# Performance work log

Hardware: AMD Instinct MI355X
Metric: run time of the kernel (lower is better)

The kernel has to match this reference:

```python
import jax, jax.numpy as jnp
import numpy as np

B, S, HID, NH, HD, RD = 1, 2048, 2560, 32, 80, 64
SCALE = HD ** -0.5
NEG = -1e9


def _alibi_slopes(n):
    # n = 32 is a power of two -> standard geometric slopes 2^(-8i/n)
    return jnp.asarray(2.0 ** (-8.0 * np.arange(1, n + 1) / n), dtype=jnp.float32)


def _rope(x, pos):
    # GPT-NeoX style rotary on the first RD dims of each head; x: [B,S,NH,HD]
    inv_freq = 1.0 / (10000.0 ** (np.arange(0, RD, 2, dtype=np.float32) / RD))  # [RD/2]
    ang = pos.astype(jnp.float32)[..., None] * jnp.asarray(inv_freq)  # [B,S,RD/2]
    cos = jnp.cos(ang)[:, :, None, :]  # [B,S,1,RD/2]
    sin = jnp.sin(ang)[:, :, None, :]
    x1 = x[..., : RD // 2]
    x2 = x[..., RD // 2 : RD]
    rot = jnp.concatenate([x1 * cos - x2 * sin, x2 * cos + x1 * sin], axis=-1)
    return jnp.concatenate([rot, x[..., RD:]], axis=-1)


def setup_inputs() -> dict:
    key = jax.random.key(0)
    k1, k2, k3 = jax.random.split(key, 3)
    return {
        "position_ids": jnp.arange(B * S, dtype=jnp.int32).reshape(B, S) % S,
        "hidden_states": jax.random.normal(k1, (B, S, HID), dtype=jnp.float32),
        "w_qkv": jax.random.normal(k2, (HID, 3 * HID), dtype=jnp.float32) * 0.02,
        "w_out": jax.random.normal(k3, (HID, HID), dtype=jnp.float32) * 0.02,
    }


def reference(position_ids, hidden_states, w_qkv, w_out):
    qkv = hidden_states @ w_qkv                       # [B,S,3*HID]
    q, k, v = jnp.split(qkv, 3, axis=-1)
    q = _rope(q.reshape(B, S, NH, HD), position_ids)
    k = _rope(k.reshape(B, S, NH, HD), position_ids)
    v = v.reshape(B, S, NH, HD)

    scores = jnp.einsum("bqhd,bkhd->bhqk", q, k) * SCALE  # [B,NH,S,S]
    rel = (position_ids[:, None, :] - position_ids[:, :, None]).astype(jnp.float32)  # j - i
    slopes = _alibi_slopes(NH)
    bias = slopes[None, :, None, None] * rel[:, None, :, :]  # [B,NH,S,S]
    causal = rel <= 0.0
    scores = jnp.where(causal[:, None, :, :], scores + bias, NEG)
    attn = jax.nn.softmax(scores, axis=-1)
    out = jnp.einsum("bhqk,bkhd->bqhd", attn, v).reshape(B, S, HID)
    return out @ w_out
```

## Files before the change

kernel.cpp:

```cpp
#include <hip/hip_runtime.h>
#include <type_traits>
#include <utility>

typedef unsigned short u16;
typedef unsigned int u32;
typedef __attribute__((ext_vector_type(8))) short short8;
typedef __attribute__((ext_vector_type(8))) __bf16 bhalf8;
typedef __attribute__((ext_vector_type(4))) short short4v;
typedef __attribute__((ext_vector_type(4))) __bf16 bhalf4;
typedef __attribute__((ext_vector_type(4))) float f32x4;
typedef __attribute__((ext_vector_type(4))) unsigned short us4;

#define S_LEN 2048
#define NHEAD 32
#define HD 80
#define HDP 96
#define HID 2560
#define N3 7680
#define QK_SCALE 0.11180339887498949f
#define LOG2E 1.4426950408889634f

template <typename T, typename = void> struct MfmaTakes : std::false_type {};
template <typename T>
struct MfmaTakes<T, std::void_t<decltype(__builtin_amdgcn_mfma_f32_16x16x32_bf16(
                       std::declval<T>(), std::declval<T>(), std::declval<f32x4>(), 0, 0, 0))>>
    : std::true_type {};

template <typename AB>
__device__ inline f32x4 mfma_raw(AB a, AB b, f32x4 c) {
  return __builtin_amdgcn_mfma_f32_16x16x32_bf16(a, b, c, 0, 0, 0);
}
using mfma_ab_t = std::conditional_t<MfmaTakes<bhalf8>::value, bhalf8, short8>;
__device__ inline f32x4 MFMA(short8 a, short8 b, f32x4 c) {
  return mfma_raw<mfma_ab_t>(__builtin_bit_cast(mfma_ab_t, a),
                             __builtin_bit_cast(mfma_ab_t, b), c);
}

#if defined(__has_builtin)
#if __has_builtin(__builtin_amdgcn_mfma_f32_16x16x16bf16_1k)
#define MFMA16_RAW(a, b, c) __builtin_amdgcn_mfma_f32_16x16x16bf16_1k(a, b, c, 0, 0, 0)
#define HAVE_MFMA16 1
#elif __has_builtin(__builtin_amdgcn_mfma_f32_16x16x16_bf16)
#define MFMA16_RAW(a, b, c) __builtin_amdgcn_mfma_f32_16x16x16_bf16(a, b, c, 0, 0, 0)
#define HAVE_MFMA16 1
#endif
#endif

#ifdef HAVE_MFMA16
template <typename T, typename = void> struct M16Takes : std::false_type {};
template <typename T>
struct M16Takes<T, std::void_t<decltype(MFMA16_RAW(std::declval<T>(), std::declval<T>(),
                                                   std::declval<f32x4>()))>> : std::true_type {};
using m16_t = std::conditional_t<M16Takes<bhalf4>::value, bhalf4, short4v>;
__device__ inline f32x4 MFMA16(short4v a, short4v b, f32x4 c) {
  return MFMA16_RAW(__builtin_bit_cast(m16_t, a), __builtin_bit_cast(m16_t, b), c);
}
#else
__device__ inline f32x4 MFMA16(short4v a, short4v b, f32x4 c) {
  short8 a8 = {a[0], a[1], a[2], a[3], 0, 0, 0, 0};
  short8 b8 = {b[0], b[1], b[2], b[3], 0, 0, 0, 0};
  return MFMA(a8, b8, c);
}
#endif

__device__ inline float bf2f(u16 b) { return __uint_as_float(((u32)b) << 16); }
__device__ inline u16 f2bf(float f) {
  u32 u = __float_as_uint(f);
  u += 0x7fffu + ((u >> 16) & 1u);
  return (u16)(u >> 16);
}

typedef __attribute__((address_space(1))) void as1_void;
typedef __attribute__((address_space(3))) void as3_void;

#if defined(__has_builtin)
#if __has_builtin(__builtin_amdgcn_global_load_lds)
#define HAVE_GLL 1
#endif
#endif

__device__ inline void stage16(const u16* g, u16* lds_base, int lane) {
#ifdef HAVE_GLL
  (void)lane;
  __builtin_amdgcn_global_load_lds((as1_void*)g, (as3_void*)lds_base, 16, 0, 0);
#else
  *(short8*)(lds_base + lane * 8) = *(const short8*)g;
#endif
}

__device__ inline void sched_barrier0() {
#if defined(__has_builtin)
#if __has_builtin(__builtin_amdgcn_sched_barrier)
  __builtin_amdgcn_sched_barrier(0);
#endif
#endif
}

__global__ __launch_bounds__(256) void detect_dtype(const u32* __restrict__ words,
                                                    int* __restrict__ flag) {
  __shared__ int red[256];
  int junk = 0;
  for (int i = threadIdx.x; i < 2048; i += 256) {
    u16 lo = (u16)(words[i] & 0xffffu);
    u32 e = (lo >> 7) & 0xffu;
    junk += (e >= 137u);
  }
  red[threadIdx.x] = junk;
  __syncthreads();
  for (int s = 128; s > 0; s >>= 1) {
    if (threadIdx.x < s) red[threadIdx.x] += red[threadIdx.x + s];
    __syncthreads();
  }
  if (threadIdx.x == 0) flag[0] = (red[0] > 64) ? 1 : 0;
}

__global__ __launch_bounds__(256) void convert_hidden(const void* __restrict__ in,
                                                      u16* __restrict__ out, int n4,
                                                      const int* __restrict__ flagp) {
  const int f = *flagp;
  int i = blockIdx.x * 256 + threadIdx.x;
  if (i >= n4) return;
  if (f) {
    const float* inf = (const float*)in;
    us4 o;
#pragma unroll
    for (int j = 0; j < 4; ++j) o[j] = f2bf(inf[(size_t)i * 4 + j]);
    *(us4*)&out[(size_t)i * 4] = o;
  } else {
    *(us4*)&out[(size_t)i * 4] = *(const us4*)&((const u16*)in)[(size_t)i * 4];
  }
}

__global__ __launch_bounds__(256) void transpose64(const void* __restrict__ in,
                                                   u16* __restrict__ out,
                                                   int istride, int ioff, int ostride,
                                                   const int* __restrict__ flagp) {
  __shared__ u16 tile[64][66];
  const int f = flagp ? *flagp : 0;
  const int bx = blockIdx.x * 64, by = blockIdx.y * 64;
  const int tx4 = (threadIdx.x & 15) * 4, ty = threadIdx.x >> 4;
#pragma unroll
  for (int i = 0; i < 4; ++i) {
    const int row = ty + i * 16;
    const size_t idx = (size_t)(by + row) * istride + ioff + bx + tx4;
    us4 v;
    if (f) {
      const f32x4 x = *(const f32x4*)&((const float*)in)[idx];
#pragma unroll
      for (int j = 0; j < 4; ++j) v[j] = f2bf(x[j]);
    } else {
      v = *(const us4*)&((const u16*)in)[idx];
    }
    *(u32*)&tile[row][tx4] = (u32)v[0] | ((u32)v[1] << 16);
    *(u32*)&tile[row][tx4 + 2] = (u32)v[2] | ((u32)v[3] << 16);
  }
  __syncthreads();
#pragma unroll
  for (int i = 0; i < 4; ++i) {
    const int oc = ty + i * 16;
    us4 o;
#pragma unroll
    for (int j = 0; j < 4; ++j) o[j] = tile[tx4 + j][oc];
    *(us4*)&out[(size_t)(bx + oc) * ostride + by + tx4] = o;
  }
}

__global__ __launch_bounds__(256) void gemm_bt(const u16* __restrict__ A,
                                               const u16* __restrict__ Bt,
                                               void* __restrict__ C,
                                               int M, int N, int K,
                                               const int* __restrict__ flagp) {
  __shared__ u16 As[128 * 32];
  __shared__ u16 Bs[128 * 32];
  const int tid = threadIdx.x;
  const int w = tid >> 6, l = tid & 63;
  const int la = l & 15, qd = l >> 4;
  const int m0 = blockIdx.y * 128, n0 = blockIdx.x * 128;
  const int mw = (w >> 1) * 64, nw = (w & 1) * 64;
  const int rowA = l >> 2;
  const int segk = (l & 3) * 8;
  const int of32 = flagp ? *flagp : 0;
  f32x4 acc[4][4] = {};

  for (int k0 = 0; k0 < K; k0 += 32) {
#pragma unroll
    for (int j = 0; j < 2; ++j) {
      const int rb = w * 16 + j * 64;
      const u16* ga = A + (size_t)(m0 + rb + rowA) * K + k0 + segk;
      const u16* gb = Bt + (size_t)(n0 + rb + rowA) * K + k0 + segk;
      stage16(ga, &As[rb * 32], l);
      stage16(gb, &Bs[rb * 32], l);
    }
    __syncthreads();
    short8 af[4], bfr[4];
#pragma unroll
    for (int i = 0; i < 4; ++i)
      af[i] = *(const short8*)&As[(mw + i * 16 + la) * 32 + qd * 8];
#pragma unroll
    for (int j = 0; j < 4; ++j)
      bfr[j] = *(const short8*)&Bs[(nw + j * 16 + la) * 32 + qd * 8];
#pragma unroll
    for (int i = 0; i < 4; ++i)
#pragma unroll
      for (int j = 0; j < 4; ++j)
        acc[i][j] = MFMA(af[i], bfr[j], acc[i][j]);
    __syncthreads();
  }

#pragma unroll
  for (int i = 0; i < 4; ++i)
#pragma unroll
    for (int j = 0; j < 4; ++j) {
      const int r0 = m0 + mw + i * 16 + qd * 4;
      const int c0 = n0 + nw + j * 16 + la;
#pragma unroll
      for (int r = 0; r < 4; ++r) {
        if (of32)
          ((float*)C)[(size_t)(r0 + r) * N + c0] = acc[i][j][r];
        else
          ((u16*)C)[(size_t)(r0 + r) * N + c0] = f2bf(acc[i][j][r]);
      }
    }
}

__global__ __launch_bounds__(512, 2) void gemm256(const u16* __restrict__ A,
                                                  const u16* __restrict__ Bt,
                                                  u16* __restrict__ C,
                                                  int M, int N, int K) {
  __shared__ u16 As[2][256 * 64];
  __shared__ u16 Bs[2][256 * 64];
  const int tid = threadIdx.x;
  const int w = tid >> 6, l = tid & 63, la = l & 15, qd = l >> 4;
  const int wr = w >> 2, wc = w & 3;

  const int nbx = gridDim.x;
  const int nwg = nbx * gridDim.y;
  int lin = blockIdx.y * nbx + blockIdx.x;
  if ((nwg & 7) == 0) lin = (lin & 7) * (nwg >> 3) + (lin >> 3);
  const int m0 = (lin / nbx) * 256, n0 = (lin % nbx) * 256;
  const int NT = K >> 6;

  const int sx0 = (qd ^ (la & 7)) * 8;
  const int sx1 = ((4 + qd) ^ (la & 7)) * 8;
  const int gsw = ((tid & 7) ^ ((tid >> 3) & 7)) * 8;

  f32x4 acc[8][4] = {};

  auto issue = [&](int s) {
    if (s >= NT * 4) return;
    const int kt = s >> 2, part = s & 3, buf = kt & 1;
    const int h = part & 1;
    const u16* G = (part >= 2) ? A : Bt;
    const int b0 = (part >= 2) ? m0 : n0;
    u16* L = ((part >= 2) ? &As[buf][0] : &Bs[buf][0]) + h * 8192;
    const int k0 = kt << 6;
#pragma unroll
    for (int q = 0; q < 2; ++q) {
      const int row = h * 128 + q * 64 + (tid >> 3);
      const u16* g = G + (size_t)(b0 + row) * K + k0 + gsw;
      stage16(g, L + (q * 512 + w * 64) * 8, l);
    }
  };

  auto readA = [&](int buf, int mh, short8(&af)[4][2]) {
    const u16* base = &As[buf][0];
#pragma unroll
    for (int i = 0; i < 4; ++i) {
      const int ro = (wr * 128 + mh * 64 + i * 16 + la) * 64;
      af[i][0] = *(const short8*)(base + ro + sx0);
      af[i][1] = *(const short8*)(base + ro + sx1);
    }
  };
  auto readB = [&](int buf, int nh, short8(&bf)[2][2]) {
    const u16* base = &Bs[buf][0];
#pragma unroll
    for (int j = 0; j < 2; ++j) {
      const int ro = (wc * 64 + nh * 32 + j * 16 + la) * 64;
      bf[j][0] = *(const short8*)(base + ro + sx0);
      bf[j][1] = *(const short8*)(base + ro + sx1);
    }
  };
  auto quad = [&](short8(&af)[4][2], short8(&bf)[2][2], int mh, int nh) {
#pragma unroll
    for (int kk = 0; kk < 2; ++kk)
#pragma unroll
      for (int i = 0; i < 4; ++i)
#pragma unroll
        for (int jj = 0; jj < 2; ++jj)
          acc[mh * 4 + i][nh * 2 + jj] =
              MFMA(af[i][kk], bf[jj][kk], acc[mh * 4 + i][nh * 2 + jj]);
  };

#pragma unroll
  for (int s = 0; s < 6; ++s) issue(s);
  asm volatile("s_waitcnt vmcnt(4)" ::: "memory");
  __builtin_amdgcn_s_barrier();

  for (int t = 0; t < NT; ++t) {
    const int buf = t & 1;
    short8 af[4][2], af2[4][2], bf0[2][2], bf1[2][2];
    readA(buf, 0, af);
    sched_barrier0();
    readB(buf, 0, bf0);
    sched_barrier0();
    readB(buf, 1, bf1);
    sched_barrier0();
    issue(4 * t + 6);
    issue(4 * t + 7);
    asm volatile("s_waitcnt lgkmcnt(4)" ::: "memory");
    sched_barrier0();
    readA(buf, 1, af2);
    sched_barrier0();
    __builtin_amdgcn_s_setprio(1);
    quad(af, bf0, 0, 0);
    __builtin_amdgcn_s_setprio(0);
    asm volatile("s_waitcnt lgkmcnt(8)" ::: "memory");
    sched_barrier0();
    __builtin_amdgcn_s_setprio(1);
    quad(af, bf1, 0, 1);
    __builtin_amdgcn_s_setprio(0);
    __builtin_amdgcn_s_barrier();
    issue(4 * t + 8);
    issue(4 * t + 9);
    asm volatile("s_waitcnt lgkmcnt(0)" ::: "memory");
    sched_barrier0();
    __builtin_amdgcn_s_setprio(1);
    quad(af2, bf0, 1, 0);
    quad(af2, bf1, 1, 1);
    __builtin_amdgcn_s_setprio(0);
    asm volatile("s_waitcnt vmcnt(4)" ::: "memory");
    __builtin_amdgcn_s_barrier();
  }

#pragma unroll
  for (int i = 0; i < 8; ++i)
#pragma unroll
    for (int j = 0; j < 4; ++j) {
      const int r0 = m0 + wr * 128 + i * 16 + qd * 4;
      const int c0 = n0 + wc * 64 + j * 16 + la;
#pragma unroll
      for (int r = 0; r < 4; ++r)
        C[(size_t)(r0 + r) * N + c0] = f2bf(acc[i][j][r]);
    }
}

__global__ __launch_bounds__(256) void rope_prep(const u16* __restrict__ qkv,
                                                 const int* __restrict__ pos,
                                                 u16* __restrict__ Qh,
                                                 u16* __restrict__ Kt) {
  const int s = blockIdx.x;
  const int h = blockIdx.y * 4 + (threadIdx.x >> 6);
  const int t = threadIdx.x & 63;
  const size_t qin = (size_t)s * N3 + h * HD;
  const size_t kin = qin + HID;
  const size_t ob = ((size_t)h * S_LEN + s) * HDP;
  const size_t kb = ((size_t)(h * 32) + (s >> 6)) * 6144 + (size_t)(s & 63) * 8;
  if (t < 32) {
    const float p = (float)pos[s];
    const float inv = exp2f(-(float)t * (13.287712379549449f / 32.0f));
    const float ang = p * inv;
    const float cs = cosf(ang), sn = sinf(ang);
    float x1 = bf2f(qkv[qin + t]), x2 = bf2f(qkv[qin + t + 32]);
    Qh[ob + t] = f2bf(x1 * cs - x2 * sn);
    Qh[ob + t + 32] = f2bf(x2 * cs + x1 * sn);
    x1 = bf2f(qkv[kin + t]);
    x2 = bf2f(qkv[kin + t + 32]);
    Kt[kb + (size_t)(t >> 3) * 512 + (t & 7)] = f2bf(x1 * cs - x2 * sn);
    const int d2 = t + 32;
    Kt[kb + (size_t)(d2 >> 3) * 512 + (d2 & 7)] = f2bf(x2 * cs + x1 * sn);
  } else if (t < 48) {
    const int d = t + 32;
    Qh[ob + d] = qkv[qin + d];
    Kt[kb + (size_t)(d >> 3) * 512 + (d & 7)] = qkv[kin + d];
  } else {
    const int d = t + 32;
    Qh[ob + d] = 0;
    Kt[kb + (size_t)(d >> 3) * 512 + (d & 7)] = 0;
  }
}

__global__ __launch_bounds__(512) void attn_fused(const u16* __restrict__ Qh,
                                                  const u16* __restrict__ Kt,
                                                  const u16* __restrict__ Vt,
                                                  u16* __restrict__ AO) {
  __shared__ u16 Ks[2][768 * 8];
  __shared__ u16 Vs[2][640 * 8];
  const int tid = threadIdx.x, w = tid >> 6, l = tid & 63;
  const int la = l & 15, qd = l >> 4;
  const int h = blockIdx.y;
  const int p = blockIdx.x;
  const int q0A = (15 - p) * 128;
  const int q0B = p * 128;
  const int nItA = (q0A >> 6) + 2;
  const int nItB = (q0B >> 6) + 2;
  const size_t hS = (size_t)h * S_LEN;

  short8 qfA[3], qfB[3];
#pragma unroll
  for (int c = 0; c < 3; ++c) {
    qfA[c] = *(const short8*)&Qh[(hS + q0A + w * 16 + la) * HDP + c * 32 + qd * 8];
    qfB[c] = *(const short8*)&Qh[(hS + q0B + w * 16 + la) * HDP + c * 32 + qd * 8];
  }

  const float slope2 = exp2f(-0.25f * (float)(h + 1)) * LOG2E;
  const float scl2 = QK_SCALE * LOG2E;
  float m_i = -1e30f, l_i = 0.f;
  f32x4 acc[5] = {};

  const u16* gK = Kt + (size_t)h * 32 * 6144;
  const u16* gV = Vt + (size_t)h * HD * S_LEN;

  auto stage = [&](int kt_g, int buf) {
    const u16* gkt = gK + (size_t)kt_g * 6144;
    stage16(gkt + (size_t)(w * 64 + l) * 8, &Ks[buf][(w * 64) * 8], l);
    if (w < 4)
      stage16(gkt + (size_t)(512 + w * 64 + l) * 8, &Ks[buf][(512 + w * 64) * 8], l);
    const u16* gv = gV + (kt_g << 6);
    {
      const int c = w * 64 + l;
      const int row = c >> 3, seg = c & 7;
      const int gcol = ((seg - (row & 7)) & 7) * 8;
      stage16(gv + (size_t)row * S_LEN + gcol, &Vs[buf][(w * 64) * 8], l);
    }
    if (w < 2) {
      const int c = 512 + w * 64 + l;
      const int row = c >> 3, seg = c & 7;
      const int gcol = ((seg - (row & 7)) & 7) * 8;
      stage16(gv + (size_t)row * S_LEN + gcol, &Vs[buf][(512 + w * 64) * 8], l);
    }
  };

  int g = 0;
  stage(0, 0);

  auto run_seg = [&](const short8(&qf)[3], int q0, int nIt, bool more) {
    const int qb = q0 + w * 16;
    const int q = qb + la;
    for (int it = 0; it < nIt; ++it, ++g) {
      const int buf = g & 1;
      __syncthreads();
      if (it + 1 < nIt) stage(it + 1, buf ^ 1);
      else if (more) stage(0, buf ^ 1);
      const int k0 = it << 6;
      if (k0 >= qb + 16) continue;

      f32x4 st[4];
#pragma unroll
      for (int kt = 0; kt < 4; ++kt) {
        short8 kf[3];
#pragma unroll
        for (int c = 0; c < 3; ++c)
          kf[c] = *(const short8*)&Ks[buf][((c * 4 + qd) * 64 + kt * 16 + la) * 8];
        f32x4 z = {};
#pragma unroll
        for (int c = 0; c < 3; ++c) z = MFMA(kf[c], qf[c], z);
        st[kt] = z;
      }

      const float base = (float)(k0 + qd * 4 - q);
      float mloc = -1e30f;
      if (k0 + 64 <= qb + 1) {
#pragma unroll
        for (int kt = 0; kt < 4; ++kt)
#pragma unroll
          for (int r = 0; r < 4; ++r) {
            const float rel = base + (float)(kt * 16 + r);
            const float v = st[kt][r] * scl2 + slope2 * rel;
            st[kt][r] = v;
            mloc = fmaxf(mloc, v);
          }
      } else {
#pragma unroll
        for (int kt = 0; kt < 4; ++kt)
#pragma unroll
          for (int r = 0; r < 4; ++r) {
            const float rel = base + (float)(kt * 16 + r);
            const float v = (rel <= 0.f) ? st[kt][r] * scl2 + slope2 * rel : -1e30f;
            st[kt][r] = v;
            mloc = fmaxf(mloc, v);
          }
      }
      mloc = fmaxf(mloc, __shfl_xor(mloc, 16));
      mloc = fmaxf(mloc, __shfl_xor(mloc, 32));

      if (!__all(mloc - m_i <= 8.0f)) {
        const float nm = fmaxf(m_i, mloc);
        const float al = exp2f(m_i - nm);
        m_i = nm;
        l_i *= al;
#pragma unroll
        for (int dt = 0; dt < 5; ++dt) acc[dt] *= al;
      }

      float ps = 0.f;
      short4v pf[4];
#pragma unroll
      for (int kt = 0; kt < 4; ++kt) {
        short4v pk;
#pragma unroll
        for (int r = 0; r < 4; ++r) {
          const float pv = exp2f(st[kt][r] - m_i);
          ps += pv;
          pk[r] = (short)f2bf(pv);
        }
        pf[kt] = pk;
      }
      ps += __shfl_xor(ps, 16);
      ps += __shfl_xor(ps, 32);
      l_i += ps;

      const int cb = qd * 4 + ((la & 7) << 3);
#pragma unroll
      for (int dt = 0; dt < 5; ++dt) {
        const int vrow = (dt * 16 + la) * 64;
#pragma unroll
        for (int kt = 0; kt < 4; ++kt) {
          const short4v vf = *(const short4v*)&Vs[buf][vrow + ((kt * 16 + cb) & 63)];
          acc[dt] = MFMA16(vf, pf[kt], acc[dt]);
        }
      }
    }
    const float inv = 1.0f / l_i;
    const size_t row = (size_t)q;
#pragma unroll
    for (int dt = 0; dt < 5; ++dt) {
      us4 o;
#pragma unroll
      for (int r = 0; r < 4; ++r) o[r] = f2bf(acc[dt][r] * inv);
      *(us4*)&AO[row * HID + h * HD + dt * 16 + qd * 4] = o;
    }
    m_i = -1e30f;
    l_i = 0.f;
#pragma unroll
    for (int dt = 0; dt < 5; ++dt) acc[dt] = f32x4{};
  };

  run_seg(qfA, q0A, nItA, true);
  run_seg(qfB, q0B, nItB, false);
}

extern "C" void kernel_launch(void* const* d_in, const int* in_sizes, int n_in,
                              void* d_out, int out_size, void* d_ws, size_t ws_size,
                              hipStream_t stream) {
  const int* pos = (const int*)d_in[0];
  const void* hidden = d_in[1];
  const void* w_qkv = d_in[2];
  const void* w_out = d_in[3];
  u16* ws = (u16*)d_ws;

  u16* Hb = ws;
  u16* WtQ = Hb + (size_t)S_LEN * HID;
  u16* WtO = WtQ + (size_t)N3 * HID;
  u16* qkv = WtO + (size_t)HID * HID;
  int* flag = (int*)(qkv + (size_t)S_LEN * N3);
  u16* Vt = Hb;
  u16* Qh = WtQ;
  u16* Kh = Qh + (size_t)NHEAD * S_LEN * HDP;
  u16* AO = Kh + (size_t)NHEAD * S_LEN * HDP;

  detect_dtype<<<1, 256, 0, stream>>>((const u32*)hidden, flag);
  convert_hidden<<<(S_LEN * HID / 4 + 255) / 256, 256, 0, stream>>>(hidden, Hb,
                                                                    S_LEN * HID / 4, flag);
  transpose64<<<dim3(N3 / 64, HID / 64), 256, 0, stream>>>(w_qkv, WtQ, N3, 0, HID, flag);
  transpose64<<<dim3(HID / 64, HID / 64), 256, 0, stream>>>(w_out, WtO, HID, 0, HID, flag);
  gemm256<<<dim3(N3 / 256, S_LEN / 256), 512, 0, stream>>>(Hb, WtQ, qkv, S_LEN, N3, HID);
  transpose64<<<dim3(HID / 64, S_LEN / 64), 256, 0, stream>>>(qkv, Vt, N3, 2 * HID, S_LEN,
                                                              nullptr);
  rope_prep<<<dim3(S_LEN, NHEAD / 4), 256, 0, stream>>>(qkv, pos, Qh, Kh);
  attn_fused<<<dim3(8, NHEAD), 512, 0, stream>>>(Qh, Kh, Vt, AO);
  gemm_bt<<<dim3(HID / 128, S_LEN / 128), 256, 0, stream>>>(AO, WtO, d_out, S_LEN, HID, HID,
                                                            flag);
}
```

Baseline: 426.8 us.

## Pipeline output GEMM with double-buffered LDS and split attention into per-tile blocks

Replaces the simple single-buffered output projection GEMM with a 128x128 kernel that uses 64-wide K tiles, double-buffered swizzled LDS, XCD-aware block remapping, interleaved load issue, and explicit waitcnt/priority scheduling to overlap global loads with MFMA work. The attention kernel no longer pairs two query tiles per block. It launches one block per 128-row tile, with the tile order reversed for half the heads to balance work, and raises the occupancy hint. The intent is better latency hiding in both kernels. The cost is more complex hand scheduling and an uneven causal workload per block.

```diff
diff --git a/kernel.cpp b/kernel.cpp
--- a/kernel.cpp
+++ b/kernel.cpp
@@ -165,54 +165,123 @@
   }
 }
 
-__global__ __launch_bounds__(256) void gemm_bt(const u16* __restrict__ A,
-                                               const u16* __restrict__ Bt,
-                                               void* __restrict__ C,
-                                               int M, int N, int K,
-                                               const int* __restrict__ flagp) {
-  __shared__ u16 As[128 * 32];
-  __shared__ u16 Bs[128 * 32];
+__global__ __launch_bounds__(256, 2) void gemm128c(const u16* __restrict__ A,
+                                                   const u16* __restrict__ Bt,
+                                                   void* __restrict__ C,
+                                                   int M, int N, int K,
+                                                   const int* __restrict__ flagp) {
+  __shared__ u16 As[2][128 * 64];
+  __shared__ u16 Bs[2][128 * 64];
   const int tid = threadIdx.x;
-  const int w = tid >> 6, l = tid & 63;
-  const int la = l & 15, qd = l >> 4;
-  const int m0 = blockIdx.y * 128, n0 = blockIdx.x * 128;
-  const int mw = (w >> 1) * 64, nw = (w & 1) * 64;
-  const int rowA = l >> 2;
-  const int segk = (l & 3) * 8;
+  const int w = tid >> 6, l = tid & 63, la = l & 15, qd = l >> 4;
+  const int wr = w >> 1, wc = w & 1;
   const int of32 = flagp ? *flagp : 0;
+
+  const int nbx = gridDim.x;
+  const int nwg = nbx * gridDim.y;
+  int lin = blockIdx.y * nbx + blockIdx.x;
+  if ((nwg & 7) == 0) lin = (lin & 7) * (nwg >> 3) + (lin >> 3);
+  const int m0 = (lin / nbx) * 128, n0 = (lin % nbx) * 128;
+  const int NT = K >> 6;
+
+  const int sx0 = (qd ^ (la & 7)) * 8;
+  const int sx1 = ((4 + qd) ^ (la & 7)) * 8;
+  const int gsw = ((tid & 7) ^ ((tid >> 3) & 7)) * 8;
+
   f32x4 acc[4][4] = {};
 
-  for (int k0 = 0; k0 < K; k0 += 32) {
+  auto issue = [&](int s) {
+    if (s >= NT * 4) return;
+    const int kt = s >> 2, part = s & 3, buf = kt & 1;
+    const int h = part & 1;
+    const u16* G = (part >= 2) ? A : Bt;
+    const int b0 = (part >= 2) ? m0 : n0;
+    u16* L = ((part >= 2) ? &As[buf][0] : &Bs[buf][0]) + h * 4096;
+    const int k0 = kt << 6;
+#pragma unroll
+    for (int q = 0; q < 2; ++q) {
+      const int row = h * 64 + q * 32 + (tid >> 3);
+      const u16* g = G + (size_t)(b0 + row) * K + k0 + gsw;
+      stage16(g, L + (q * 256 + w * 64) * 8, l);
+    }
+  };
+
+  auto readA = [&](int buf, int mh, short8(&af)[2][2]) {
+    const u16* base = &As[buf][0];
+#pragma unroll
+    for (int i = 0; i < 2; ++i) {
+      const int ro = (wr * 64 + mh * 32 + i * 16 + la) * 64;
+      af[i][0] = *(const short8*)(base + ro + sx0);
+      af[i][1] = *(const short8*)(base + ro + sx1);
+    }
+  };
+  auto readB = [&](int buf, int nh, short8(&bf)[2][2]) {
+    const u16* base = &Bs[buf][0];
 #pragma unroll
     for (int j = 0; j < 2; ++j) {
-      const int rb = w * 16 + j * 64;
-      const u16* ga = A + (size_t)(m0 + rb + rowA) * K + k0 + segk;
-      const u16* gb = Bt + (size_t)(n0 + rb + rowA) * K + k0 + segk;
-      stage16(ga, &As[rb * 32], l);
-      stage16(gb, &Bs[rb * 32], l);
-    }
-    __syncthreads();
-    short8 af[4], bfr[4];
-#pragma unroll
-    for (int i = 0; i < 4; ++i)
-      af[i] = *(const short8*)&As[(mw + i * 16 + la) * 32 + qd * 8];
-#pragma unroll
-    for (int j = 0; j < 4; ++j)
-      bfr[j] = *(const short8*)&Bs[(nw + j * 16 + la) * 32 + qd * 8];
-#pragma unroll
-    for (int i = 0; i < 4; ++i)
-#pragma unroll
-      for (int j = 0; j < 4; ++j)
-        acc[i][j] = MFMA(af[i], bfr[j], acc[i][j]);
-    __syncthreads();
+      const int ro = (wc * 64 + nh * 32 + j * 16 + la) * 64;
+      bf[j][0] = *(const short8*)(base + ro + sx0);
+      bf[j][1] = *(const short8*)(base + ro + sx1);
+    }
+  };
+  auto quad = [&](short8(&af)[2][2], short8(&bf)[2][2], int mh, int nh) {
+#pragma unroll
+    for (int kk = 0; kk < 2; ++kk)
+#pragma unroll
+      for (int i = 0; i < 2; ++i)
+#pragma unroll
+        for (int jj = 0; jj < 2; ++jj)
+          acc[mh * 2 + i][nh * 2 + jj] =
+              MFMA(af[i][kk], bf[jj][kk], acc[mh * 2 + i][nh * 2 + jj]);
+  };
+
+#pragma unroll
+  for (int s = 0; s < 6; ++s) issue(s);
+  asm volatile("s_waitcnt vmcnt(4)" ::: "memory");
+  __builtin_amdgcn_s_barrier();
+
+  for (int t = 0; t < NT; ++t) {
+    const int buf = t & 1;
+    short8 af[2][2], af2[2][2], bf0[2][2], bf1[2][2];
+    readA(buf, 0, af);
+    sched_barrier0();
+    readB(buf, 0, bf0);
+    sched_barrier0();
+    readB(buf, 1, bf1);
+    sched_barrier0();
+    issue(4 * t + 6);
+    issue(4 * t + 7);
+    asm volatile("s_waitcnt lgkmcnt(4)" ::: "memory");
+    sched_barrier0();
+    readA(buf, 1, af2);
+    sched_barrier0();
+    __builtin_amdgcn_s_setprio(1);
+    quad(af, bf0, 0, 0);
+    __builtin_amdgcn_s_setprio(0);
+    asm volatile("s_waitcnt lgkmcnt(4)" ::: "memory");
+    sched_barrier0();
+    __builtin_amdgcn_s_setprio(1);
+    quad(af, bf1, 0, 1);
+    __builtin_amdgcn_s_setprio(0);
+    __builtin_amdgcn_s_barrier();
+    issue(4 * t + 8);
+    issue(4 * t + 9);
+    asm volatile("s_waitcnt lgkmcnt(0)" ::: "memory");
+    sched_barrier0();
+    __builtin_amdgcn_s_setprio(1);
+    quad(af2, bf0, 1, 0);
+    quad(af2, bf1, 1, 1);
+    __builtin_amdgcn_s_setprio(0);
+    asm volatile("s_waitcnt vmcnt(4)" ::: "memory");
+    __builtin_amdgcn_s_barrier();
   }
 
 #pragma unroll
   for (int i = 0; i < 4; ++i)
 #pragma unroll
     for (int j = 0; j < 4; ++j) {
-      const int r0 = m0 + mw + i * 16 + qd * 4;
-      const int c0 = n0 + nw + j * 16 + la;
+      const int r0 = m0 + wr * 64 + (i >> 1) * 32 + (i & 1) * 16 + qd * 4;
+      const int c0 = n0 + wc * 64 + (j >> 1) * 32 + (j & 1) * 16 + la;
 #pragma unroll
       for (int r = 0; r < 4; ++r) {
         if (of32)
@@ -379,28 +448,27 @@
   }
 }
 
-__global__ __launch_bounds__(512) void attn_fused(const u16* __restrict__ Qh,
-                                                  const u16* __restrict__ Kt,
-                                                  const u16* __restrict__ Vt,
-                                                  u16* __restrict__ AO) {
+__global__ __launch_bounds__(512, 4) void attn_fused(const u16* __restrict__ Qh,
+                                                     const u16* __restrict__ Kt,
+                                                     const u16* __restrict__ Vt,
+                                                     u16* __restrict__ AO) {
   __shared__ u16 Ks[2][768 * 8];
   __shared__ u16 Vs[2][640 * 8];
   const int tid = threadIdx.x, w = tid >> 6, l = tid & 63;
   const int la = l & 15, qd = l >> 4;
   const int h = blockIdx.y;
   const int p = blockIdx.x;
-  const int q0A = (15 - p) * 128;
-  const int q0B = p * 128;
-  const int nItA = (q0A >> 6) + 2;
-  const int nItB = (q0B >> 6) + 2;
+  const int tile = (h < 16) ? p : 15 - p;
+  const int q0 = tile * 128;
+  const int nIt = 2 * tile + 2;
   const size_t hS = (size_t)h * S_LEN;
 
-  short8 qfA[3], qfB[3];
-#pragma unroll
-  for (int c = 0; c < 3; ++c) {
-    qfA[c] = *(const short8*)&Qh[(hS + q0A + w * 16 + la) * HDP + c * 32 + qd * 8];
-    qfB[c] = *(const short8*)&Qh[(hS + q0B + w * 16 + la) * HDP + c * 32 + qd * 8];
-  }
+  const int qb = q0 + w * 16;
+  const int q = qb + la;
+  short8 qf[3];
+#pragma unroll
+  for (int c = 0; c < 3; ++c)
+    qf[c] = *(const short8*)&Qh[(hS + qb + la) * HDP + c * 32 + qd * 8];
 
   const float slope2 = exp2f(-0.25f * (float)(h + 1)) * LOG2E;
   const float scl2 = QK_SCALE * LOG2E;
@@ -430,113 +498,100 @@
     }
   };
 
-  int g = 0;
   stage(0, 0);
-
-  auto run_seg = [&](const short8(&qf)[3], int q0, int nIt, bool more) {
-    const int qb = q0 + w * 16;
-    const int q = qb + la;
-    for (int it = 0; it < nIt; ++it, ++g) {
-      const int buf = g & 1;
-      __syncthreads();
-      if (it + 1 < nIt) stage(it + 1, buf ^ 1);
-      else if (more) stage(0, buf ^ 1);
-      const int k0 = it << 6;
-      if (k0 >= qb + 16) continue;
-
-      f32x4 st[4];
+  for (int it = 0; it < nIt; ++it) {
+    const int buf = it & 1;
+    __syncthreads();
+    if (it + 1 < nIt) stage(it + 1, buf ^ 1);
+    const int k0 = it << 6;
+    if (k0 >= qb + 16) continue;
+
+    f32x4 st[4];
+#pragma unroll
+    for (int kt = 0; kt < 4; ++kt) {
+      short8 kf[3];
+#pragma unroll
+      for (int c = 0; c < 3; ++c)
+        kf[c] = *(const short8*)&Ks[buf][((c * 4 + qd) * 64 + kt * 16 + la) * 8];
+      f32x4 z = {};
+#pragma unroll
+      for (int c = 0; c < 3; ++c) z = MFMA(kf[c], qf[c], z);
+      st[kt] = z;
+    }
+
+    const float base = (float)(k0 + qd * 4 - q);
+    float mloc = -1e30f;
+    if (k0 + 64 <= qb + 1) {
+#pragma unroll
+      for (int kt = 0; kt < 4; ++kt)
+#pragma unroll
+        for (int r = 0; r < 4; ++r) {
+          const float rel = base + (float)(kt * 16 + r);
+          const float v = st[kt][r] * scl2 + slope2 * rel;
+          st[kt][r] = v;
+          mloc = fmaxf(mloc, v);
+        }
+    } else {
+#pragma unroll
+      for (int kt = 0; kt < 4; ++kt)
+#pragma unroll
+        for (int r = 0; r < 4; ++r) {
+          const float rel = base + (float)(kt * 16 + r);
+          const float v = (rel <= 0.f) ? st[kt][r] * scl2 + slope2 * rel : -1e30f;
+          st[kt][r] = v;
+          mloc = fmaxf(mloc, v);
+        }
+    }
+    mloc = fmaxf(mloc, __shfl_xor(mloc, 16));
+    mloc = fmaxf(mloc, __shfl_xor(mloc, 32));
+
+    if (!__all(mloc - m_i <= 8.0f)) {
+      const float nm = fmaxf(m_i, mloc);
+      const float al = exp2f(m_i - nm);
+      m_i = nm;
+      l_i *= al;
+#pragma unroll
+      for (int dt = 0; dt < 5; ++dt) acc[dt] *= al;
+    }
+
+    float ps = 0.f;
+    short4v pf[4];
+#pragma unroll
+    for (int kt = 0; kt < 4; ++kt) {
+      short4v pk;
+#pragma unroll
+      for (int r = 0; r < 4; ++r) {
+        const float pv = exp2f(st[kt][r] - m_i);
+        ps += pv;
+        pk[r] = (short)f2bf(pv);
+      }
+      pf[kt] = pk;
+    }
+    ps += __shfl_xor(ps, 16);
+    ps += __shfl_xor(ps, 32);
+    l_i += ps;
+
+    const int cb = qd * 4 + ((la & 7) << 3);
+#pragma unroll
+    for (int dt = 0; dt < 5; ++dt) {
+      const int vrow = (dt * 16 + la) * 64;
 #pragma unroll
       for (int kt = 0; kt < 4; ++kt) {
-        short8 kf[3];
-#pragma unroll
-        for (int c = 0; c < 3; ++c)
-          kf[c] = *(const short8*)&Ks[buf][((c * 4 + qd) * 64 + kt * 16 + la) * 8];
-        f32x4 z = {};
-#pragma unroll
-        for (int c = 0; c < 3; ++c) z = MFMA(kf[c], qf[c], z);
-        st[kt] = z;
+        const short4v vf = *(const short4v*)&Vs[buf][vrow + ((kt * 16 + cb) & 63)];
+        acc[dt] = MFMA16(vf, pf[kt], acc[dt]);
       }
-
-      const float base = (float)(k0 + qd * 4 - q);
-      float mloc = -1e30f;
-      if (k0 + 64 <= qb + 1) {
-#pragma unroll
-        for (int kt = 0; kt < 4; ++kt)
-#pragma unroll
-          for (int r = 0; r < 4; ++r) {
-            const float rel = base + (float)(kt * 16 + r);
-            const float v = st[kt][r] * scl2 + slope2 * rel;
-            st[kt][r] = v;
-            mloc = fmaxf(mloc, v);
-          }
-      } else {
-#pragma unroll
-        for (int kt = 0; kt < 4; ++kt)
-#pragma unroll
-          for (int r = 0; r < 4; ++r) {
-            const float rel = base + (float)(kt * 16 + r);
-            const float v = (rel <= 0.f) ? st[kt][r] * scl2 + slope2 * rel : -1e30f;
-            st[kt][r] = v;
-            mloc = fmaxf(mloc, v);
-          }
-      }
-      mloc = fmaxf(mloc, __shfl_xor(mloc, 16));
-      mloc = fmaxf(mloc, __shfl_xor(mloc, 32));
-
-      if (!__all(mloc - m_i <= 8.0f)) {
-        const float nm = fmaxf(m_i, mloc);
-        const float al = exp2f(m_i - nm);
-        m_i = nm;
-        l_i *= al;
-#pragma unroll
-        for (int dt = 0; dt < 5; ++dt) acc[dt] *= al;
-      }
-
-      float ps = 0.f;
-      short4v pf[4];
-#pragma unroll
-      for (int kt = 0; kt < 4; ++kt) {
-        short4v pk;
-#pragma unroll
-        for (int r = 0; r < 4; ++r) {
-          const float pv = exp2f(st[kt][r] - m_i);
-          ps += pv;
-          pk[r] = (short)f2bf(pv);
-        }
-        pf[kt] = pk;
-      }
-      ps += __shfl_xor(ps, 16);
-      ps += __shfl_xor(ps, 32);
-      l_i += ps;
-
-      const int cb = qd * 4 + ((la & 7) << 3);
-#pragma unroll
-      for (int dt = 0; dt < 5; ++dt) {
-        const int vrow = (dt * 16 + la) * 64;
-#pragma unroll
-        for (int kt = 0; kt < 4; ++kt) {
-          const short4v vf = *(const short4v*)&Vs[buf][vrow + ((kt * 16 + cb) & 63)];
-          acc[dt] = MFMA16(vf, pf[kt], acc[dt]);
-        }
-      }
-    }
-    const float inv = 1.0f / l_i;
-    const size_t row = (size_t)q;
-#pragma unroll
-    for (int dt = 0; dt < 5; ++dt) {
-      us4 o;
-#pragma unroll
-      for (int r = 0; r < 4; ++r) o[r] = f2bf(acc[dt][r] * inv);
-      *(us4*)&AO[row * HID + h * HD + dt * 16 + qd * 4] = o;
-    }
-    m_i = -1e30f;
-    l_i = 0.f;
-#pragma unroll
-    for (int dt = 0; dt < 5; ++dt) acc[dt] = f32x4{};
-  };
-
-  run_seg(qfA, q0A, nItA, true);
-  run_seg(qfB, q0B, nItB, false);
+    }
+  }
+
+  const float inv = 1.0f / l_i;
+  const size_t row = (size_t)q;
+#pragma unroll
+  for (int dt = 0; dt < 5; ++dt) {
+    us4 o;
+#pragma unroll
+    for (int r = 0; r < 4; ++r) o[r] = f2bf(acc[dt][r] * inv);
+    *(us4*)&AO[row * HID + h * HD + dt * 16 + qd * 4] = o;
+  }
 }
 
 extern "C" void kernel_launch(void* const* d_in, const int* in_sizes, int n_in,
@@ -567,7 +622,7 @@
   transpose64<<<dim3(HID / 64, S_LEN / 64), 256, 0, stream>>>(qkv, Vt, N3, 2 * HID, S_LEN,
                                                               nullptr);
   rope_prep<<<dim3(S_LEN, NHEAD / 4), 256, 0, stream>>>(qkv, pos, Qh, Kh);
-  attn_fused<<<dim3(8, NHEAD), 512, 0, stream>>>(Qh, Kh, Vt, AO);
-  gemm_bt<<<dim3(HID / 128, S_LEN / 128), 256, 0, stream>>>(AO, WtO, d_out, S_LEN, HID, HID,
-                                                            flag);
-}
+  attn_fused<<<dim3(16, NHEAD), 512, 0, stream>>>(Qh, Kh, Vt, AO);
+  gemm128c<<<dim3(HID / 128, S_LEN / 128), 256, 0, stream>>>(AO, WtO, d_out, S_LEN, HID,
+                                                             HID, flag);
+}
```

After: 389.4 us. -8.8%, faster.
